# Performance work log

Measured on AMD Instinct MI355X. Metric: run time of the kernel, lower is better.

## Reference

```python
import jax, jax.numpy as jnp
import numpy as np
from jax import lax

TOTAL_LENGTH = 1024
EMBED_DIM = 128
GRAPH_DIM = 50257
N_STEP = 128  # min_len
BATCH = 32


def setup_inputs() -> dict:
    key = jax.random.key(0)
    k1, k2, k3, k4, k5, k6, k7 = jax.random.split(key, 7)
    s_e = 1.0 / np.sqrt(EMBED_DIM)
    return {
        "zi": jax.random.randint(k1, (BATCH,), 0, TOTAL_LENGTH),
        "y": jax.random.randint(k2, (BATCH, N_STEP), 0, GRAPH_DIM),
        "latent": jax.random.normal(k3, (TOTAL_LENGTH, EMBED_DIM), dtype=jnp.float32) * s_e,
        "Wt": jax.random.normal(k4, (EMBED_DIM, EMBED_DIM), dtype=jnp.float32) * s_e,
        "bt": jax.random.normal(k5, (EMBED_DIM,), dtype=jnp.float32) * s_e,
        "Wv": jax.random.normal(k6, (GRAPH_DIM, EMBED_DIM), dtype=jnp.float32) * s_e,
        "bv": jax.random.normal(k7, (GRAPH_DIM,), dtype=jnp.float32) * s_e,
    }


def reference(zi, y, latent, Wt, bt, Wv, bv):
    # z0: [B, E] gathered from latent table
    z0 = latent[zi]

    def step(z, _):
        # emit current z, then update: z <- tanh(z + transition(z))
        z_next = jnp.tanh(z + z @ Wt.T + bt)
        return z_next, z

    _, zs = lax.scan(step, z0, None, length=N_STEP)  # [T, B, E]
    zs = jnp.transpose(zs, (1, 0, 2))                # [B, T, E]
    logits = jnp.einsum("bte,ve->btv", zs, Wv) + bv  # [B, T, V]
    ys = jax.nn.log_softmax(logits, axis=-1)
    yp = jnp.take_along_axis(ys, y[:, :, None], axis=-1)[:, :, 0]  # [B, T]
    return yp
```

## Files before the change

### kernel.cpp

```cpp
#include <hip/hip_runtime.h>
#include <hip/hip_bf16.h>
#include <hip/hip_fp8.h>

#define EMBED 128
#define TSTEPS 128
#define NBATCH 32
#define VDIM 50257
#define VPAD 50304
#define MROWS 4096
#define NGROUPS 786
#define GRIDX 64
#define GRIDY 16
#define MAXGRP 13
#define CONV_N4 ((VDIM * EMBED) / 4)
#define CONV_BLOCKS ((CONV_N4 + 255) / 256)

static constexpr float LOG2E = 1.4426950408889634f;
static constexpr float LN2   = 0.6931471805599453f;

__device__ __forceinline__ float fast_exp2(float x) {
#if __has_builtin(__builtin_amdgcn_exp2f)
    return __builtin_amdgcn_exp2f(x);
#else
    return exp2f(x);
#endif
}
__device__ __forceinline__ float fast_log2(float x) {
#if __has_builtin(__builtin_amdgcn_logf)
    return __builtin_amdgcn_logf(x);
#else
    return log2f(x);
#endif
}
__device__ __forceinline__ float fast_rcp(float x) {
#if __has_builtin(__builtin_amdgcn_rcpf)
    return __builtin_amdgcn_rcpf(x);
#else
    return 1.0f / x;
#endif
}
__device__ __forceinline__ float fast_tanh_nr(float x) {
    x = fminf(20.0f, fmaxf(-20.0f, x));
    float t = fast_exp2((2.0f * LOG2E) * x);
    float u = t + 1.0f;
    float r = fast_rcp(u);
    r = r * fmaf(-u, r, 2.0f);
    return (t - 1.0f) * r;
}
__device__ __forceinline__ unsigned short f2bf_raw(float f) {
    __hip_bfloat16 h = __float2bfloat16(f);
    union { __hip_bfloat16 b; unsigned short u; } cvt;
    cvt.b = h;
    return cvt.u;
}
__device__ __forceinline__ float bf_raw2f(unsigned short u) {
    union { unsigned int u; float f; } cvt;
    cvt.u = ((unsigned int)u) << 16;
    return cvt.f;
}
template <bool HI>
__device__ __forceinline__ int pk_fp8(float a, float b, int old) {
#if __has_builtin(__builtin_amdgcn_cvt_pk_fp8_f32)
    return __builtin_amdgcn_cvt_pk_fp8_f32(a, b, old, HI);
#else
    __hip_fp8_e4m3 x(a), y(b);
    int v = (int)(unsigned char)x.__x | ((int)(unsigned char)y.__x << 8);
    return HI ? ((old & 0xffff) | (v << 16)) : ((old & ~0xffff) | v);
#endif
}

__global__ __launch_bounds__(256) void setup_kernel(const int* __restrict__ zi,
                                                    const float* __restrict__ latent,
                                                    const float* __restrict__ Wt,
                                                    const float* __restrict__ bt,
                                                    const float* __restrict__ Wv,
                                                    const float* __restrict__ bv,
                                                    unsigned short* __restrict__ zsb,
                                                    unsigned char* __restrict__ zsa8,
                                                    unsigned char* __restrict__ wv8,
                                                    float* __restrict__ bvs,
                                                    float* __restrict__ S) {
    if (blockIdx.x >= NBATCH) {
        const int cb = blockIdx.x - NBATCH;
        if (cb == 0) {
#pragma unroll
            for (int i = 0; i < MROWS / 256; i++)
                S[i * 256 + threadIdx.x] = 0.f;
        }
        if (cb == 1) {
            const int base  = VDIM * EMBED / 4;
            const int npad  = (VPAD - VDIM) * EMBED / 4;
            for (int i = threadIdx.x; i < npad; i += 256)
                reinterpret_cast<unsigned int*>(wv8)[base + i] = 0u;
        }
        const int idx = cb * 256 + threadIdx.x;
        if (idx < VPAD)
            bvs[idx] = (idx < VDIM) ? bv[idx] * LOG2E : -1e30f;
        if (idx < CONV_N4) {
            float4 v = reinterpret_cast<const float4*>(Wv)[idx];
            int p = pk_fp8<false>(v.x, v.y, 0);
            p = pk_fp8<true>(v.z, v.w, p);
            reinterpret_cast<unsigned int*>(wv8)[idx] = (unsigned int)p;
        }
        return;
    }

    __shared__ float zbuf[2][EMBED];
    __shared__ unsigned short zstash[TSTEPS * EMBED];
    const int b = blockIdx.x;
    const int e = threadIdx.x >> 1;
    const int h = threadIdx.x & 1;

    float4 wrow[16];
    const float4* wt4 = reinterpret_cast<const float4*>(Wt + e * EMBED + h * 64);
#pragma unroll
    for (int i = 0; i < 16; i++) wrow[i] = wt4[i];
    const float bte = bt[e];

    if (h == 0) zbuf[0][e] = latent[zi[b] * EMBED + e];
    __syncthreads();

    int cur = 0;
    for (int t = 0; t < TSTEPS; t++) {
        const float zc = zbuf[cur][e];
        if (h == 0)
            zstash[t * EMBED + e] = f2bf_raw(zc * LOG2E);

        const float4* z4 = reinterpret_cast<const float4*>(&zbuf[cur][h * 64]);
        float4 acc = {0.f, 0.f, 0.f, 0.f};
#pragma unroll
        for (int i = 0; i < 16; i++) {
            float4 zv = z4[i];
            acc.x += zv.x * wrow[i].x;
            acc.y += zv.y * wrow[i].y;
            acc.z += zv.z * wrow[i].z;
            acc.w += zv.w * wrow[i].w;
        }
        float v = acc.x + acc.y + acc.z + acc.w;
        float p = __shfl_xor(v, 1);
        float sA = h ? p : v;
        float sB = h ? v : p;
        float znew = fast_tanh_nr(((zc + sA) + sB) + bte);
        if (h == 0) zbuf[cur ^ 1][e] = znew;
        __syncthreads();
        cur ^= 1;
    }

    uint4* dstb = reinterpret_cast<uint4*>(zsb + (long)b * TSTEPS * EMBED);
    uint2* dsta = reinterpret_cast<uint2*>(zsa8 + (long)b * TSTEPS * EMBED);
    const uint4* src = reinterpret_cast<const uint4*>(zstash);
    for (int i = threadIdx.x; i < TSTEPS * EMBED / 8; i += 256) {
        uint4 w = src[i];
        dstb[i] = w;
        float f0 = bf_raw2f(w.x & 0xffff), f1 = bf_raw2f(w.x >> 16);
        float f2 = bf_raw2f(w.y & 0xffff), f3 = bf_raw2f(w.y >> 16);
        float f4 = bf_raw2f(w.z & 0xffff), f5 = bf_raw2f(w.z >> 16);
        float f6 = bf_raw2f(w.w & 0xffff), f7 = bf_raw2f(w.w >> 16);
        int lo = pk_fp8<false>(f0, f1, 0); lo = pk_fp8<true>(f2, f3, lo);
        int hi = pk_fp8<false>(f4, f5, 0); hi = pk_fp8<true>(f6, f7, hi);
        uint2 o; o.x = (unsigned int)lo; o.y = (unsigned int)hi;
        dsta[i] = o;
    }
}

typedef __attribute__((ext_vector_type(4))) float f32x4;

__global__ __launch_bounds__(256) void gemm_lse_kernel(const unsigned char* __restrict__ zsa8,
                                                       const unsigned char* __restrict__ wv8,
                                                       const float* __restrict__ bvs,
                                                       float* __restrict__ S) {
    __shared__ unsigned char ldsb[2][8192];
    __shared__ float ldsbias[MAXGRP * 64];

    const int lane  = threadIdx.x & 63;
    const int wave  = threadIdx.x >> 6;
    const int col16 = lane & 15;
    const int quad  = lane >> 4;
    const int mbase = blockIdx.y * 256 + wave * 64;

    const int x  = blockIdx.x;
    const int g0 = x * 12 + min(x, 18);
    const int g1 = g0 + 12 + (x < 18 ? 1 : 0);
    const int nbias = (g1 - g0) * 64;

    for (int i = threadIdx.x; i < nbias; i += 256)
        ldsbias[i] = bvs[g0 * 64 + i];

    unsigned long long a[4][4];
#pragma unroll
    for (int s = 0; s < 4; s++)
#pragma unroll
        for (int c = 0; c < 4; c++)
            a[s][c] = *reinterpret_cast<const unsigned long long*>(
                zsa8 + (long)(mbase + s * 16 + col16) * EMBED + c * 32 + quad * 8);

    float sums[16];
#pragma unroll
    for (int i = 0; i < 16; i++) sums[i] = 0.f;

    auto stage = [&](int buf, int g) {
#pragma unroll
        for (int j = 0; j < 2; j++) {
            const int rr = (wave * 2 + j) * 8 + (lane >> 3);
            const int G  = (lane & 7) ^ (rr & 7);
            const unsigned char* gp = wv8 + (long)(g * 64 + rr) * EMBED + G * 16;
            __builtin_amdgcn_global_load_lds(
                (const __attribute__((address_space(1))) void*)gp,
                (__attribute__((address_space(3))) void*)&ldsb[buf][(wave * 2 + j) * 1024],
                16, 0, 0);
        }
    };

    int cur = 0;
    stage(0, g0);

    const f32x4 dzero = {0.f, 0.f, 0.f, 0.f};

    for (int g = g0; g < g1; g++) {
        __syncthreads();
        if (g + 1 < g1) stage(cur ^ 1, g + 1);

        const float* biasg = &ldsbias[(g - g0) * 64];

#pragma unroll
        for (int c = 0; c < 4; c++) {
            const unsigned char* rowp = &ldsb[cur][(c * 16 + col16) * 128];
            const int r7 = col16 & 7;
            unsigned long long bf[4];
#pragma unroll
            for (int kc = 0; kc < 4; kc++) {
                const int q_abs = kc * 4 + quad;
                bf[kc] = *reinterpret_cast<const unsigned long long*>(
                    rowp + (((q_abs >> 1) ^ r7) * 16) + ((q_abs & 1) * 8));
            }

            const float eb = fast_exp2(biasg[c * 16 + col16]);

            f32x4 d[4];
#pragma unroll
            for (int s = 0; s < 4; s++)
                d[s] = __builtin_amdgcn_mfma_f32_16x16x32_fp8_fp8(
                    (long long)a[s][0], (long long)bf[0], dzero, 0, 0, 0);
#pragma unroll
            for (int kc = 1; kc < 4; kc++)
#pragma unroll
                for (int s = 0; s < 4; s++)
                    d[s] = __builtin_amdgcn_mfma_f32_16x16x32_fp8_fp8(
                        (long long)a[s][kc], (long long)bf[kc], d[s], 0, 0, 0);

#pragma unroll
            for (int s = 0; s < 4; s++)
#pragma unroll
                for (int r = 0; r < 4; r++)
                    sums[s * 4 + r] = fmaf(fast_exp2(d[s][r]), eb, sums[s * 4 + r]);
        }
        cur ^= 1;
    }

#pragma unroll
    for (int s = 0; s < 4; s++) {
#pragma unroll
        for (int r = 0; r < 4; r++) {
            float v = sums[s * 4 + r];
            v += __shfl_xor(v, 1);
            v += __shfl_xor(v, 2);
            v += __shfl_xor(v, 4);
            v += __shfl_xor(v, 8);
            if (col16 == 0)
                atomicAdd(&S[mbase + s * 16 + quad * 4 + r], v);
        }
    }
}

__global__ __launch_bounds__(256) void tail_kernel(const unsigned short* __restrict__ zsb,
                                                   const float* __restrict__ Wv,
                                                   const float* __restrict__ bv,
                                                   const int* __restrict__ y,
                                                   const float* __restrict__ S,
                                                   float* __restrict__ out) {
    const int row  = blockIdx.x * 4 + (threadIdx.x >> 6);
    const int lane = threadIdx.x & 63;
    const int yv = y[row];
    const ushort2* zr = reinterpret_cast<const ushort2*>(zsb + (long)row * EMBED);
    const float2*  wr = reinterpret_cast<const float2*>(Wv + (long)yv * EMBED);
    ushort2 z2 = zr[lane];
    float2  w2 = wr[lane];
    float v = bf_raw2f(z2.x) * w2.x + bf_raw2f(z2.y) * w2.y;
    v += __shfl_xor(v, 32);
    v += __shfl_xor(v, 16);
    v += __shfl_xor(v, 8);
    v += __shfl_xor(v, 4);
    v += __shfl_xor(v, 2);
    v += __shfl_xor(v, 1);
    if (lane == 0)
        out[row] = LN2 * (v - fast_log2(S[row])) + bv[yv];
}

extern "C" void kernel_launch(void* const* d_in, const int* in_sizes, int n_in,
                              void* d_out, int out_size, void* d_ws, size_t ws_size,
                              hipStream_t stream) {
    const int*   zi     = (const int*)d_in[0];
    const int*   y      = (const int*)d_in[1];
    const float* latent = (const float*)d_in[2];
    const float* Wt     = (const float*)d_in[3];
    const float* bt     = (const float*)d_in[4];
    const float* Wv     = (const float*)d_in[5];
    const float* bv     = (const float*)d_in[6];
    float* out = (float*)d_out;

    char* ws = (char*)d_ws;
    unsigned short* zsb  = (unsigned short*)ws;
    unsigned char*  zsa8 = (unsigned char*)(ws + (1u << 20));
    float*          S    = (float*)(ws + 1536u * 1024);
    float*          bvs  = (float*)(ws + 1536u * 1024 + (64u << 10));
    unsigned char*  wv8  = (unsigned char*)(ws + (2u << 20));

    setup_kernel<<<NBATCH + CONV_BLOCKS, 256, 0, stream>>>(zi, latent, Wt, bt, Wv, bv,
                                                           zsb, zsa8, wv8, bvs, S);

    gemm_lse_kernel<<<dim3(GRIDX, GRIDY), 256, 0, stream>>>(zsa8, wv8, bvs, S);

    tail_kernel<<<MROWS / 4, 256, 0, stream>>>(zsb, Wv, bv, y, S, out);
}
```

Measured before the change: 196.7 us.

## Pack two batch scans per block and double GEMM grid width

The recurrent scan now runs two batch elements per 256-thread block, with each thread computing a full 128-wide dot product instead of splitting it across a lane pair with a shuffle. This halves the number of scan blocks. The GEMM grid is widened from 64 to 128 column blocks, each handling about half as many vocab groups, to raise occupancy. The trade-off is a longer serial dot product per thread and more register pressure in the scan, and the wider GEMM reloads the A fragments and bias more often across blocks.

```diff
diff --git a/kernel.cpp b/kernel.cpp
--- a/kernel.cpp
+++ b/kernel.cpp
@@ -5,13 +5,14 @@
 #define EMBED 128
 #define TSTEPS 128
 #define NBATCH 32
+#define SCANB 16
 #define VDIM 50257
 #define VPAD 50304
 #define MROWS 4096
 #define NGROUPS 786
-#define GRIDX 64
+#define GRIDX 128
 #define GRIDY 16
-#define MAXGRP 13
+#define MAXGRP 7
 #define CONV_N4 ((VDIM * EMBED) / 4)
 #define CONV_BLOCKS ((CONV_N4 + 255) / 256)
 
@@ -80,8 +81,8 @@
                                                     unsigned char* __restrict__ wv8,
                                                     float* __restrict__ bvs,
                                                     float* __restrict__ S) {
-    if (blockIdx.x >= NBATCH) {
-        const int cb = blockIdx.x - NBATCH;
+    if (blockIdx.x >= SCANB) {
+        const int cb = blockIdx.x - SCANB;
         if (cb == 0) {
 #pragma unroll
             for (int i = 0; i < MROWS / 256; i++)
@@ -105,51 +106,60 @@
         return;
     }
 
-    __shared__ float zbuf[2][EMBED];
-    __shared__ unsigned short zstash[TSTEPS * EMBED];
-    const int b = blockIdx.x;
-    const int e = threadIdx.x >> 1;
-    const int h = threadIdx.x & 1;
-
-    float4 wrow[16];
-    const float4* wt4 = reinterpret_cast<const float4*>(Wt + e * EMBED + h * 64);
-#pragma unroll
-    for (int i = 0; i < 16; i++) wrow[i] = wt4[i];
+    __shared__ float zbuf[2][2][EMBED];
+    __shared__ unsigned short zstash[2][TSTEPS * EMBED];
+    const int j = threadIdx.x >> 7;
+    const int e = threadIdx.x & 127;
+    const int b = blockIdx.x * 2 + j;
+
+    float4 wrowA[16], wrowB[16];
+    const float4* wt4 = reinterpret_cast<const float4*>(Wt + e * EMBED);
+#pragma unroll
+    for (int i = 0; i < 16; i++) wrowA[i] = wt4[i];
+#pragma unroll
+    for (int i = 0; i < 16; i++) wrowB[i] = wt4[16 + i];
     const float bte = bt[e];
 
-    if (h == 0) zbuf[0][e] = latent[zi[b] * EMBED + e];
+    zbuf[j][0][e] = latent[zi[b] * EMBED + e];
     __syncthreads();
 
     int cur = 0;
     for (int t = 0; t < TSTEPS; t++) {
-        const float zc = zbuf[cur][e];
-        if (h == 0)
-            zstash[t * EMBED + e] = f2bf_raw(zc * LOG2E);
-
-        const float4* z4 = reinterpret_cast<const float4*>(&zbuf[cur][h * 64]);
-        float4 acc = {0.f, 0.f, 0.f, 0.f};
+        const float zc = zbuf[j][cur][e];
+        zstash[j][t * EMBED + e] = f2bf_raw(zc * LOG2E);
+
+        const float4* z4 = reinterpret_cast<const float4*>(&zbuf[j][cur][0]);
+        float4 accA = {0.f, 0.f, 0.f, 0.f};
 #pragma unroll
         for (int i = 0; i < 16; i++) {
             float4 zv = z4[i];
-            acc.x += zv.x * wrow[i].x;
-            acc.y += zv.y * wrow[i].y;
-            acc.z += zv.z * wrow[i].z;
-            acc.w += zv.w * wrow[i].w;
-        }
-        float v = acc.x + acc.y + acc.z + acc.w;
-        float p = __shfl_xor(v, 1);
-        float sA = h ? p : v;
-        float sB = h ? v : p;
-        float znew = fast_tanh_nr(((zc + sA) + sB) + bte);
-        if (h == 0) zbuf[cur ^ 1][e] = znew;
+            accA.x += zv.x * wrowA[i].x;
+            accA.y += zv.y * wrowA[i].y;
+            accA.z += zv.z * wrowA[i].z;
+            accA.w += zv.w * wrowA[i].w;
+        }
+        float vA = accA.x + accA.y + accA.z + accA.w;
+        float4 accB = {0.f, 0.f, 0.f, 0.f};
+#pragma unroll
+        for (int i = 0; i < 16; i++) {
+            float4 zv = z4[16 + i];
+            accB.x += zv.x * wrowB[i].x;
+            accB.y += zv.y * wrowB[i].y;
+            accB.z += zv.z * wrowB[i].z;
+            accB.w += zv.w * wrowB[i].w;
+        }
+        float vB = accB.x + accB.y + accB.z + accB.w;
+
+        float znew = fast_tanh_nr(((zc + vA) + vB) + bte);
+        zbuf[j][cur ^ 1][e] = znew;
         __syncthreads();
         cur ^= 1;
     }
 
     uint4* dstb = reinterpret_cast<uint4*>(zsb + (long)b * TSTEPS * EMBED);
     uint2* dsta = reinterpret_cast<uint2*>(zsa8 + (long)b * TSTEPS * EMBED);
-    const uint4* src = reinterpret_cast<const uint4*>(zstash);
-    for (int i = threadIdx.x; i < TSTEPS * EMBED / 8; i += 256) {
+    const uint4* src = reinterpret_cast<const uint4*>(&zstash[j][0]);
+    for (int i = e; i < TSTEPS * EMBED / 8; i += 128) {
         uint4 w = src[i];
         dstb[i] = w;
         float f0 = bf_raw2f(w.x & 0xffff), f1 = bf_raw2f(w.x >> 16);
@@ -179,8 +189,8 @@
     const int mbase = blockIdx.y * 256 + wave * 64;
 
     const int x  = blockIdx.x;
-    const int g0 = x * 12 + min(x, 18);
-    const int g1 = g0 + 12 + (x < 18 ? 1 : 0);
+    const int g0 = x * 6 + min(x, 18);
+    const int g1 = g0 + 6 + (x < 18 ? 1 : 0);
     const int nbias = (g1 - g0) * 64;
 
     for (int i = threadIdx.x; i < nbias; i += 256)
@@ -315,8 +325,8 @@
     float*          bvs  = (float*)(ws + 1536u * 1024 + (64u << 10));
     unsigned char*  wv8  = (unsigned char*)(ws + (2u << 20));
 
-    setup_kernel<<<NBATCH + CONV_BLOCKS, 256, 0, stream>>>(zi, latent, Wt, bt, Wv, bv,
-                                                           zsb, zsa8, wv8, bvs, S);
+    setup_kernel<<<SCANB + CONV_BLOCKS, 256, 0, stream>>>(zi, latent, Wt, bt, Wv, bv,
+                                                          zsb, zsa8, wv8, bvs, S);
 
     gemm_lse_kernel<<<dim3(GRIDX, GRIDY), 256, 0, stream>>>(zsa8, wv8, bvs, S);
 
```

Result: slower. 242.1 us (+23.1%).
